# Kernel optimization log

Measured on AMD Instinct MI355X. Metric: run time of the kernel, lower is better.

## Reference

```python
import jax, jax.numpy as jnp
import numpy as np

BL = 512  # block length (matches init bl)


def _conv1x1(w, b, x):
    # w: (out, in), b: (out,), x: (batch, in, L) -> (batch, out, L)
    return jnp.einsum('oi,bil->bol', w, x) + b[None, :, None]


def _window_mask(bl):
    # Faithful to torch loop: window_mask[:, :, i:i+bl] = 1 for i in range(bl)
    # -> all ones except the last column.
    wm = np.zeros((1, bl, bl + 2 * (bl // 2)), np.float32)
    for i in range(bl):
        wm[:, :, i:i + bl] = 1.0
    return jnp.asarray(wm)


def setup_inputs() -> dict:
    key = jax.random.key(0)
    ks = jax.random.split(key, 5)
    B, C, L = 1, 2048, 16384
    Cq = C // 2  # r1 = r2 = r3 = 2
    s_in = 1.0 / float(np.sqrt(C))
    s_mid = 1.0 / float(np.sqrt(Cq))
    return {
        'x1': jax.random.normal(ks[0], (B, C, L), jnp.float32),
        'x2': jnp.zeros((B, C, L), jnp.float32),
        'mask': jnp.ones((B, 1, L), jnp.float32),
        'wq': jax.random.normal(ks[1], (Cq, C), jnp.float32) * s_in,
        'bq': jnp.zeros((Cq,), jnp.float32),
        'wk': jax.random.normal(ks[2], (Cq, C), jnp.float32) * s_in,
        'bk': jnp.zeros((Cq,), jnp.float32),
        'wv': jax.random.normal(ks[3], (Cq, C), jnp.float32) * s_in,
        'bv': jnp.zeros((Cq,), jnp.float32),
        'wo': jax.random.normal(ks[4], (C, Cq), jnp.float32) * s_mid,
        'bo': jnp.zeros((C,), jnp.float32),
    }


def reference(x1, x2, mask, wq, bq, wk, bk, wv, bv, wo, bo):
    B, C, L = x1.shape  # B == 1 (asserted by sliding path)
    bl = BL
    nb = L // bl  # L % bl == 0 by construction
    half = bl // 2

    q = _conv1x1(wq, bq, x1)  # (1, c, L)
    k = _conv1x1(wk, bk, x1)
    v = _conv1x1(wv, bv, x1)  # encoder stage: value from x1 (x2 unused)
    c = q.shape[1]

    # query blocks: (nb, c, bl)
    qb = q.reshape(B, c, nb, bl).transpose(0, 2, 1, 3).reshape(nb, c, bl)

    # pad k/v/padding_mask with bl//2 zeros on both sides, then take overlapping
    # windows of width 2*bl per block.
    kp = jnp.pad(k, ((0, 0), (0, 0), (half, half)))[0]            # (c, L+bl)
    vp = jnp.pad(v, ((0, 0), (0, 0), (half, half)))[0]
    pm = jnp.pad(mask[:, 0:1, :], ((0, 0), (0, 0), (half, half)))[0]  # (1, L+bl)
    cols = np.arange(nb)[:, None] * bl + np.arange(2 * bl)[None, :]   # (nb, 2bl)
    kb = kp[:, cols].transpose(1, 0, 2)   # (nb, c, 2bl)
    vb = vp[:, cols].transpose(1, 0, 2)   # (nb, c, 2bl)
    pmb = pm[:, cols].transpose(1, 0, 2)  # (nb, 1, 2bl)

    final_mask = _window_mask(bl) * pmb   # (nb, bl, 2bl)

    # scalar dot attention with log-mask (as in AttentionHelper.scalar_dot_att)
    energy = jnp.einsum('ncl,ncm->nlm', qb, kb) / jnp.float32(np.sqrt(c))
    attn = jax.nn.softmax(energy + jnp.log(final_mask + 1e-9), axis=-1)
    attn = attn * final_mask
    out = jnp.einsum('ncm,nlm->ncl', vb, attn)  # (nb, c, bl)

    out = _conv1x1(wo, bo, jax.nn.relu(out))    # (nb, C, bl)
    out = out.reshape(B, nb, C, bl).transpose(0, 2, 1, 3).reshape(B, C, nb * bl)
    out = out[:, :, :L]
    return out * mask[:, 0:1, :]
```

## Files before the change

kernel.cpp:

```cpp
#include <hip/hip_runtime.h>
#include <hip/hip_bf16.h>

typedef __attribute__((ext_vector_type(4))) float f32x4;
typedef __attribute__((ext_vector_type(8))) __bf16 bf16x8;

struct ushort4_t { unsigned short x, y, z, w; };

#define DEVINL static __device__ __forceinline__

DEVINL unsigned short f2bf(float f) {
  union { float f; unsigned u; } x; x.f = f;
  return (unsigned short)((x.u + 0x7FFFu + ((x.u >> 16) & 1u)) >> 16);
}

DEVINL void gload16(const void* g, void* l) {
  __builtin_amdgcn_global_load_lds((const __attribute__((address_space(1))) void*)g,
                                   (__attribute__((address_space(3))) void*)l,
                                   16, 0, 0);
}

#define SBAR()   asm volatile("s_barrier" ::: "memory")
#define LGKM0()  asm volatile("s_waitcnt lgkmcnt(0)" ::: "memory")
#define VM(n)    asm volatile("s_waitcnt vmcnt(" #n ")" ::: "memory")

__global__ __launch_bounds__(256) void transpose_x_k(const float* __restrict__ x,
                                                     unsigned short* __restrict__ xT) {
  __shared__ float tile[32][33];
  const int bx = blockIdx.x;
  const int by = blockIdx.y;
  const int tx = threadIdx.x;
  const int ty = threadIdx.y;
#pragma unroll
  for (int i = 0; i < 4; ++i) {
    int c = by * 32 + ty + i * 8;
    tile[ty + i * 8][tx] = x[(long)c * 16384 + bx * 32 + tx];
  }
  __syncthreads();
  const int t = ty * 32 + tx;
  const int lrow = t >> 3;
  const int cq = (t & 7) << 2;
  ushort4_t o;
  o.x = f2bf(tile[cq + 0][lrow]);
  o.y = f2bf(tile[cq + 1][lrow]);
  o.z = f2bf(tile[cq + 2][lrow]);
  o.w = f2bf(tile[cq + 3][lrow]);
  *reinterpret_cast<ushort4_t*>(xT + (long)(bx * 32 + lrow) * 2048 + by * 32 + cq) = o;
}

__global__ __launch_bounds__(256) void conv_w_k(const float* __restrict__ wq,
                                                const float* __restrict__ wk,
                                                const float* __restrict__ wv,
                                                const float* __restrict__ wo,
                                                unsigned short* __restrict__ Wqk,
                                                unsigned short* __restrict__ Wv,
                                                unsigned short* __restrict__ Wo) {
  long i = ((long)blockIdx.x * 256 + threadIdx.x) * 4;
  const float* src;
  unsigned short* dst;
  if (i < 4194304) {
    src = (i < 2097152) ? (wq + i) : (wk + i - 2097152);
    dst = Wqk + i;
  } else if (i < 6291456) {
    src = wv + (i - 4194304);
    dst = Wv + (i - 4194304);
  } else {
    src = wo + (i - 6291456);
    dst = Wo + (i - 6291456);
  }
  float4 v = *reinterpret_cast<const float4*>(src);
  ushort4_t o{f2bf(v.x), f2bf(v.y), f2bf(v.z), f2bf(v.w)};
  *reinterpret_cast<ushort4_t*>(dst) = o;
}

enum { EPI_QK = 0, EPI_V = 1, EPI_S = 2, EPI_PV = 3, EPI_OUT = 4 };

struct GArgs {
  const unsigned short* A;
  const unsigned short* Bt;
  void* C;
  const float* bias;
  const float* bias2;
  const float* mask;
  const unsigned short* guard;
  int aBatch, cBatch;
  int btRow0, btRow0Step, btRowLim;
  int btK0, btK0Step, btKLim;
};

template <int EPI, int GUARDED, int LDA, int LDB, int LDC, int KK>
__global__ __launch_bounds__(512, 2) void gemm8_k(GArgs g) {
  constexpr int NK = KK >> 6;
  constexpr int NT = NK >> 1;
  __shared__ char lds[131072];

  const int t = threadIdx.x;
  const int l = t & 63;
  const int w = t >> 6;

  const int gx = gridDim.x, gxy = gx * gridDim.y;
  const int nwg = gxy * gridDim.z;
  int lin = blockIdx.z * gxy + blockIdx.y * gx + blockIdx.x;
  lin = (lin & 7) * (nwg >> 3) + (lin >> 3);
  const int z = lin / gxy;
  const int rres = lin - z * gxy;
  const int Mbase = (rres / gx) << 8;
  const int Nbase = (rres - (rres / gx) * gx) << 8;

  const int wr = w >> 2;
  const int wc = w & 3;
  const int fr = l & 15;
  const int fg = l >> 4;

  const unsigned short* Ab = g.A + (long)z * g.aBatch + (long)Mbase * LDA;
  const int bRowBase = g.btRow0 + z * g.btRow0Step + Nbase;
  const int bK0 = g.btK0 + z * g.btK0Step;

  const int rr = t >> 3;
  const int cb8s = t & 7;

  auto stage = [&](int bufSel, int unit, int kt) {
    const int k0 = (kt & (NK - 1)) << 6;
    const bool isA = (unit == 0) || (unit == 3);
#pragma unroll
    for (int gph = 0; gph < 2; ++gph) {
      int row;
      if (isA) row = (unit == 0 ? 0 : 64) + (gph << 7) + rr;
      else     row = (unit == 1 ? 0 : 32) + (gph << 7) + (rr & 31) + ((rr >> 5) << 6);
      const int cbL = cb8s ^ (row & 7);
      const int gk = k0 + (cbL << 3);
      char* lp = lds + (bufSel << 16) + (isA ? 0 : 32768) + row * 128 + (cb8s << 4);
      const char* gp;
      if (isA) {
        gp = (const char*)(Ab + (long)row * LDA + gk);
      } else if (!GUARDED) {
        gp = (const char*)(g.Bt + (long)(bRowBase + row) * LDB + (bK0 + gk));
      } else {
        const int grow = bRowBase + row;
        const int gkk = bK0 + gk;
        if ((unsigned)grow < (unsigned)g.btRowLim && (unsigned)gkk < (unsigned)g.btKLim)
          gp = (const char*)(g.Bt + (long)grow * LDB + gkk);
        else
          gp = (const char*)g.guard + (l << 4);
      }
      gload16(gp, lp);
    }
  };

  const int arow = (wr << 7) + fr;
  const int brow = (wc << 6) + fr;

  auto ldA = [&](int i8, int kk, int bufSel) -> bf16x8 {
    const int row = arow + (i8 << 4);
    const int cb = ((kk << 2) | fg) ^ (row & 7);
    return *(const bf16x8*)(lds + (bufSel << 16) + row * 128 + (cb << 4));
  };
  auto ldB = [&](int j, int kk, int bufSel) -> bf16x8 {
    const int row = brow + (j << 4);
    const int cb = ((kk << 2) | fg) ^ (row & 7);
    return *(const bf16x8*)(lds + (bufSel << 16) + 32768 + row * 128 + (cb << 4));
  };

  f32x4 acc[8][4];
#pragma unroll
  for (int i = 0; i < 8; ++i)
#pragma unroll
    for (int j = 0; j < 4; ++j) acc[i][j] = f32x4{0.f, 0.f, 0.f, 0.f};

  stage(0, 0, 0); stage(0, 1, 0); stage(0, 2, 0); stage(0, 3, 0);
  stage(1, 0, 1); stage(1, 1, 1); stage(1, 2, 1); stage(1, 3, 1);
  VM(12);
  SBAR();

  bf16x8 fa[4][2], fb[4][2];

#define MFMA_Q(QI, QJ)                                                        \
  __builtin_amdgcn_s_setprio(1);                                              \
  _Pragma("unroll") for (int kk = 0; kk < 2; ++kk)                            \
  _Pragma("unroll") for (int i = 0; i < 4; ++i)                               \
  _Pragma("unroll") for (int j = 0; j < 2; ++j)                               \
    acc[(QI)*4 + i][(QJ)*2 + j] = __builtin_amdgcn_mfma_f32_16x16x32_bf16(    \
        fa[i][kk], fb[(QJ)*2 + j][kk], acc[(QI)*4 + i][(QJ)*2 + j], 0, 0, 0); \
  __builtin_amdgcn_s_setprio(0);

#pragma unroll 1
  for (int it = 0; it < NT; ++it) {
    const int ktn0 = 2 * it + 2;
    const int ktn1 = 2 * it + 3;
#pragma unroll
    for (int i = 0; i < 4; ++i) { fa[i][0] = ldA(i, 0, 0); fa[i][1] = ldA(i, 1, 0); }
#pragma unroll
    for (int j = 0; j < 2; ++j) { fb[j][0] = ldB(j, 0, 0); fb[j][1] = ldB(j, 1, 0); }
    SBAR(); LGKM0();
    MFMA_Q(0, 0);
    VM(10); SBAR();
#pragma unroll
    for (int j = 2; j < 4; ++j) { fb[j][0] = ldB(j, 0, 0); fb[j][1] = ldB(j, 1, 0); }
    stage(0, 0, ktn0); stage(0, 1, ktn0);
    SBAR(); LGKM0();
    MFMA_Q(0, 1);
    VM(12); SBAR();
#pragma unroll
    for (int i = 0; i < 4; ++i) { fa[i][0] = ldA(4 + i, 0, 0); fa[i][1] = ldA(4 + i, 1, 0); }
    stage(0, 2, ktn0);
    SBAR(); LGKM0();
    MFMA_Q(1, 0);
    SBAR();
    stage(0, 3, ktn0);
    SBAR();
    MFMA_Q(1, 1);
    VM(12); SBAR();
#pragma unroll
    for (int i = 0; i < 4; ++i) { fa[i][0] = ldA(i, 0, 1); fa[i][1] = ldA(i, 1, 1); }
#pragma unroll
    for (int j = 0; j < 2; ++j) { fb[j][0] = ldB(j, 0, 1); fb[j][1] = ldB(j, 1, 1); }
    SBAR(); LGKM0();
    MFMA_Q(0, 0);
    VM(10); SBAR();
#pragma unroll
    for (int j = 2; j < 4; ++j) { fb[j][0] = ldB(j, 0, 1); fb[j][1] = ldB(j, 1, 1); }
    stage(1, 0, ktn1); stage(1, 1, ktn1);
    SBAR(); LGKM0();
    MFMA_Q(0, 1);
    VM(12); SBAR();
#pragma unroll
    for (int i = 0; i < 4; ++i) { fa[i][0] = ldA(4 + i, 0, 1); fa[i][1] = ldA(4 + i, 1, 1); }
    stage(1, 1 + 1, ktn1);
    SBAR(); LGKM0();
    MFMA_Q(1, 0);
    SBAR();
    stage(1, 3, ktn1);
    SBAR();
    MFMA_Q(1, 1);
    VM(12); SBAR();
  }
  VM(0); LGKM0(); SBAR();

#pragma unroll
  for (int ii = 0; ii < 8; ++ii)
#pragma unroll
    for (int j = 0; j < 4; ++j)
#pragma unroll
      for (int r = 0; r < 4; ++r) {
        const int row = Mbase + (wr << 7) + ii * 16 + fg * 4 + r;
        const int col = Nbase + (wc << 6) + j * 16 + fr;
        float val = acc[ii][j][r];
        const long off = (long)z * g.cBatch + (long)row * LDC + col;
        if (EPI == EPI_QK) {
          val = (col < 1024) ? (val + g.bias[col]) * 0.03125f
                             : (val + g.bias2[col - 1024]);
          ((unsigned short*)g.C)[off] = f2bf(val);
        } else if (EPI == EPI_V) {
          val += g.bias[row];
          ((unsigned short*)g.C)[off] = f2bf(val);
        } else if (EPI == EPI_S) {
          ((float*)g.C)[off] = val;
        } else if (EPI == EPI_PV) {
          val = fmaxf(val, 0.f);
          ((unsigned short*)g.C)[off] = f2bf(val);
        } else {
          val = (val + g.bias[row]) * g.mask[col];
          ((float*)g.C)[off] = val;
        }
      }
#undef MFMA_Q
}

__global__ __launch_bounds__(256) void softmax_k(const float* __restrict__ S,
                                                 const float* __restrict__ mask,
                                                 unsigned short* __restrict__ P) {
  const int row = blockIdx.x;
  const int n = row >> 9;
  const float* s = S + (long)row * 1024;
  unsigned short* p = P + (long)row * 1024;
  const int t = threadIdx.x;

  const float4 sv = *reinterpret_cast<const float4*>(s + t * 4);
  const int pos0 = (n << 9) + t * 4 - 256;
  float4 mv = {0.f, 0.f, 0.f, 0.f};
  if ((unsigned)pos0 < 16384u) mv = *reinterpret_cast<const float4*>(mask + pos0);
  float fm[4] = {mv.x, mv.y, mv.z, mv.w};
  if (t == 255) fm[3] = 0.f;
  const float sc[4] = {sv.x, sv.y, sv.z, sv.w};

  float logit[4];
  float lmax = -3.0e38f;
#pragma unroll
  for (int k = 0; k < 4; ++k) {
    logit[k] = sc[k] + logf(fm[k] + 1e-9f);
    lmax = fmaxf(lmax, logit[k]);
  }
#pragma unroll
  for (int o = 32; o; o >>= 1) lmax = fmaxf(lmax, __shfl_xor(lmax, o, 64));
  __shared__ float red[8];
  const int wv_ = t >> 6, ln = t & 63;
  if (ln == 0) red[wv_] = lmax;
  __syncthreads();
  const float gmax = fmaxf(fmaxf(red[0], red[1]), fmaxf(red[2], red[3]));

  float e[4], lsum = 0.f;
#pragma unroll
  for (int k = 0; k < 4; ++k) { e[k] = expf(logit[k] - gmax); lsum += e[k]; }
#pragma unroll
  for (int o = 32; o; o >>= 1) lsum += __shfl_xor(lsum, o, 64);
  if (ln == 0) red[4 + wv_] = lsum;
  __syncthreads();
  const float inv = 1.f / ((red[4] + red[5]) + (red[6] + red[7]));
  ushort4_t o4;
  o4.x = f2bf(e[0] * inv * fm[0]);
  o4.y = f2bf(e[1] * inv * fm[1]);
  o4.z = f2bf(e[2] * inv * fm[2]);
  o4.w = f2bf(e[3] * inv * fm[3]);
  *reinterpret_cast<ushort4_t*>(p + t * 4) = o4;
}

extern "C" void kernel_launch(void* const* d_in, const int* in_sizes, int n_in,
                              void* d_out, int out_size, void* d_ws, size_t ws_size,
                              hipStream_t stream) {
  const float* x1 = (const float*)d_in[0];
  const float* mask = (const float*)d_in[2];
  const float* wq = (const float*)d_in[3];
  const float* bq = (const float*)d_in[4];
  const float* wk = (const float*)d_in[5];
  const float* bk = (const float*)d_in[6];
  const float* wv = (const float*)d_in[7];
  const float* bv = (const float*)d_in[8];
  const float* wo = (const float*)d_in[9];
  const float* bo = (const float*)d_in[10];

  char* ws = (char*)d_ws;
  unsigned short* xT   = (unsigned short*)(ws);
  unsigned short* attT = xT;
  unsigned short* Wqk  = (unsigned short*)(ws + 67108864);
  unsigned short* Wv   = (unsigned short*)(ws + 75497472);
  unsigned short* Wo   = (unsigned short*)(ws + 79691776);
  unsigned short* qkT  = (unsigned short*)(ws + 83886080);
  unsigned short* vbuf = (unsigned short*)(ws + 150994944);
  float*          Sbuf = (float*)(ws + 184549376);
  unsigned short* P    = (unsigned short*)(ws + 251658240);
  unsigned short* guard= (unsigned short*)(ws + 285212672);

  hipMemsetAsync(guard, 0, 4096, stream);

  transpose_x_k<<<dim3(512, 64), dim3(32, 8), 0, stream>>>(x1, xT);
  conv_w_k<<<dim3(8192), dim3(256), 0, stream>>>(wq, wk, wv, wo, Wqk, Wv, Wo);

  const int BIG = 0x40000000;
  {
    GArgs a{};
    a.A = xT; a.Bt = Wqk; a.C = qkT;
    a.bias = bq; a.bias2 = bk; a.guard = guard;
    a.aBatch = 0; a.cBatch = 0;
    a.btRow0 = 0; a.btRow0Step = 0; a.btRowLim = BIG;
    a.btK0 = 0; a.btK0Step = 0; a.btKLim = BIG;
    gemm8_k<EPI_QK, 0, 2048, 2048, 2048, 2048><<<dim3(8, 64, 1), 512, 0, stream>>>(a);
  }
  {
    GArgs a{};
    a.A = Wv; a.Bt = xT; a.C = vbuf;
    a.bias = bv; a.guard = guard;
    a.aBatch = 0; a.cBatch = 0;
    a.btRow0 = 0; a.btRow0Step = 0; a.btRowLim = BIG;
    a.btK0 = 0; a.btK0Step = 0; a.btKLim = BIG;
    gemm8_k<EPI_V, 0, 2048, 2048, 16384, 2048><<<dim3(64, 4, 1), 512, 0, stream>>>(a);
  }
  {
    GArgs a{};
    a.A = qkT; a.Bt = qkT; a.C = Sbuf;
    a.guard = guard;
    a.aBatch = 512 * 2048; a.cBatch = 512 * 1024;
    a.btRow0 = -256; a.btRow0Step = 512; a.btRowLim = 16384;
    a.btK0 = 1024; a.btK0Step = 0; a.btKLim = BIG;
    gemm8_k<EPI_S, 1, 2048, 2048, 1024, 1024><<<dim3(4, 2, 32), 512, 0, stream>>>(a);
  }
  softmax_k<<<dim3(16384), dim3(256), 0, stream>>>(Sbuf, mask, P);
  {
    GArgs a{};
    a.A = P; a.Bt = vbuf; a.C = attT;
    a.guard = guard;
    a.aBatch = 512 * 1024; a.cBatch = 512 * 1024;
    a.btRow0 = 0; a.btRow0Step = 0; a.btRowLim = BIG;
    a.btK0 = -256; a.btK0Step = 512; a.btKLim = 16384;
    gemm8_k<EPI_PV, 1, 1024, 16384, 1024, 1024><<<dim3(4, 2, 32), 512, 0, stream>>>(a);
  }
  {
    GArgs a{};
    a.A = Wo; a.Bt = attT; a.C = d_out;
    a.bias = bo; a.mask = mask; a.guard = guard;
    a.aBatch = 0; a.cBatch = 0;
    a.btRow0 = 0; a.btRow0Step = 0; a.btRowLim = BIG;
    a.btK0 = 0; a.btK0Step = 0; a.btKLim = BIG;
    gemm8_k<EPI_OUT, 0, 1024, 1024, 16384, 1024><<<dim3(64, 8, 1), 512, 0, stream>>>(a);
  }
  (void)in_sizes; (void)n_in; (void)out_size; (void)ws_size;
}
```

Before: 462.3 us.

## Restructure GEMM main loop with fewer barriers and partial LDS waits

Replaces the manually doubled k-loop with a single per-k-tile loop that alternates buffers by parity. It issues all B fragment reads up front, uses partial lgkmcnt waits and sched_barrier to pin the order, and cuts the s_barrier count per tile. Global-to-LDS staging is regrouped into two pairs of stages with vmcnt(8) waits. This aims to raise MFMA issue density and reduce sync stalls, but it risks LDS read/write races if the remaining barriers do not protect the overwritten buffer.

```diff
diff --git a/kernel.cpp b/kernel.cpp
--- a/kernel.cpp
+++ b/kernel.cpp
@@ -20,8 +20,9 @@
 }
 
 #define SBAR()   asm volatile("s_barrier" ::: "memory")
-#define LGKM0()  asm volatile("s_waitcnt lgkmcnt(0)" ::: "memory")
+#define LGKM(n)  asm volatile("s_waitcnt lgkmcnt(" #n ")" ::: "memory")
 #define VM(n)    asm volatile("s_waitcnt vmcnt(" #n ")" ::: "memory")
+#define SCHED0() __builtin_amdgcn_sched_barrier(0)
 
 __global__ __launch_bounds__(256) void transpose_x_k(const float* __restrict__ x,
                                                      unsigned short* __restrict__ xT) {
@@ -90,7 +91,6 @@
 template <int EPI, int GUARDED, int LDA, int LDB, int LDC, int KK>
 __global__ __launch_bounds__(512, 2) void gemm8_k(GArgs g) {
   constexpr int NK = KK >> 6;
-  constexpr int NT = NK >> 1;
   __shared__ char lds[131072];
 
   const int t = threadIdx.x;
@@ -166,11 +166,6 @@
 #pragma unroll
     for (int j = 0; j < 4; ++j) acc[i][j] = f32x4{0.f, 0.f, 0.f, 0.f};
 
-  stage(0, 0, 0); stage(0, 1, 0); stage(0, 2, 0); stage(0, 3, 0);
-  stage(1, 0, 1); stage(1, 1, 1); stage(1, 2, 1); stage(1, 3, 1);
-  VM(12);
-  SBAR();
-
   bf16x8 fa[4][2], fb[4][2];
 
 #define MFMA_Q(QI, QJ)                                                        \
@@ -182,58 +177,38 @@
         fa[i][kk], fb[(QJ)*2 + j][kk], acc[(QI)*4 + i][(QJ)*2 + j], 0, 0, 0); \
   __builtin_amdgcn_s_setprio(0);
 
+  stage(0, 0, 0); stage(0, 1, 0); stage(0, 2, 0); stage(0, 3, 0);
+  stage(1, 0, 1); stage(1, 1, 1); stage(1, 2, 1); stage(1, 3, 1);
+  VM(8);
+  SBAR();
+
 #pragma unroll 1
-  for (int it = 0; it < NT; ++it) {
-    const int ktn0 = 2 * it + 2;
-    const int ktn1 = 2 * it + 3;
-#pragma unroll
-    for (int i = 0; i < 4; ++i) { fa[i][0] = ldA(i, 0, 0); fa[i][1] = ldA(i, 1, 0); }
-#pragma unroll
-    for (int j = 0; j < 2; ++j) { fb[j][0] = ldB(j, 0, 0); fb[j][1] = ldB(j, 1, 0); }
-    SBAR(); LGKM0();
+  for (int kt = 0; kt < NK; ++kt) {
+    const int cur = kt & 1;
+    const int ktn = kt + 2;
+#pragma unroll
+    for (int i = 0; i < 4; ++i) { fa[i][0] = ldA(i, 0, cur); fa[i][1] = ldA(i, 1, cur); }
+#pragma unroll
+    for (int j = 0; j < 2; ++j) { fb[j][0] = ldB(j, 0, cur); fb[j][1] = ldB(j, 1, cur); }
+    SCHED0();
+#pragma unroll
+    for (int j = 2; j < 4; ++j) { fb[j][0] = ldB(j, 0, cur); fb[j][1] = ldB(j, 1, cur); }
+    LGKM(4); SCHED0();
     MFMA_Q(0, 0);
-    VM(10); SBAR();
-#pragma unroll
-    for (int j = 2; j < 4; ++j) { fb[j][0] = ldB(j, 0, 0); fb[j][1] = ldB(j, 1, 0); }
-    stage(0, 0, ktn0); stage(0, 1, ktn0);
-    SBAR(); LGKM0();
+    SBAR();
+    stage(cur, 0, ktn); stage(cur, 1, ktn);
+    LGKM(0); SCHED0();
     MFMA_Q(0, 1);
-    VM(12); SBAR();
-#pragma unroll
-    for (int i = 0; i < 4; ++i) { fa[i][0] = ldA(4 + i, 0, 0); fa[i][1] = ldA(4 + i, 1, 0); }
-    stage(0, 2, ktn0);
-    SBAR(); LGKM0();
+#pragma unroll
+    for (int i = 0; i < 4; ++i) { fa[i][0] = ldA(4 + i, 0, cur); fa[i][1] = ldA(4 + i, 1, cur); }
+    LGKM(0); SCHED0();
     MFMA_Q(1, 0);
     SBAR();
-    stage(0, 3, ktn0);
-    SBAR();
+    stage(cur, 2, ktn); stage(cur, 3, ktn);
     MFMA_Q(1, 1);
-    VM(12); SBAR();
-#pragma unroll
-    for (int i = 0; i < 4; ++i) { fa[i][0] = ldA(i, 0, 1); fa[i][1] = ldA(i, 1, 1); }
-#pragma unroll
-    for (int j = 0; j < 2; ++j) { fb[j][0] = ldB(j, 0, 1); fb[j][1] = ldB(j, 1, 1); }
-    SBAR(); LGKM0();
-    MFMA_Q(0, 0);
-    VM(10); SBAR();
-#pragma unroll
-    for (int j = 2; j < 4; ++j) { fb[j][0] = ldB(j, 0, 1); fb[j][1] = ldB(j, 1, 1); }
-    stage(1, 0, ktn1); stage(1, 1, ktn1);
-    SBAR(); LGKM0();
-    MFMA_Q(0, 1);
-    VM(12); SBAR();
-#pragma unroll
-    for (int i = 0; i < 4; ++i) { fa[i][0] = ldA(4 + i, 0, 1); fa[i][1] = ldA(4 + i, 1, 1); }
-    stage(1, 1 + 1, ktn1);
-    SBAR(); LGKM0();
-    MFMA_Q(1, 0);
-    SBAR();
-    stage(1, 3, ktn1);
-    SBAR();
-    MFMA_Q(1, 1);
-    VM(12); SBAR();
-  }
-  VM(0); LGKM0(); SBAR();
+    VM(8); SBAR();
+  }
+  VM(0); LGKM(0); SBAR();
 
 #pragma unroll
   for (int ii = 0; ii < 8; ++ii)
```

Measured after the change: 467.0 us. Within noise of the previous version (+1.0%).
